# Optimization experiments

Measured on AMD Instinct MI355X. Metric: run time of the kernel, lower is better.

## Reference

```python
import jax, jax.numpy as jnp
import numpy as np

N = [50000, 100000, 100000, 40000, 20000]  # cells per rank 0..4
C = 64
DEG = 8
N_LAYERS = 3
PAIRS = [(0,0),(1,1),(2,2),(3,3),(4,4),(0,1),(0,2),(0,3),(0,4),(1,2),(1,3),(1,4),(2,3),(2,4),(3,4)]
E_SIZES = [DEG * N[j] for (_, j) in PAIRS]
OFF = np.concatenate([[0], np.cumsum(E_SIZES)]).astype(np.int64)
IN1 = C * 5 * 4 + 4  # 5 ranks pooled x 4 aggregators + global features


def setup_inputs() -> dict:
    key = jax.random.key(0)
    ks = jax.random.split(key, 64)
    inp = {}
    for r in range(5):
        inp[f'x_{r}'] = jax.random.normal(ks[r], (N[r], C), jnp.float32)
    rows_l, cols_l = [], []
    for k, (i, j) in enumerate(PAIRS):
        E = E_SIZES[k]
        rows_l.append(jnp.sort(jax.random.randint(ks[5 + k], (E,), 0, N[j], jnp.int32)))
        cols_l.append(jax.random.randint(ks[25 + k], (E,), 0, N[i], jnp.int32))
    inp['rows'] = jnp.concatenate(rows_l)
    inp['cols'] = jnp.concatenate(cols_l)
    inp['vals'] = jax.random.uniform(ks[41], (int(OFF[-1]),), jnp.float32) * 0.1
    inp['global_feature'] = jax.random.normal(ks[42], (1, 4), jnp.float32)
    inp['W_hmc'] = jax.random.normal(ks[43], (N_LAYERS, 15, C, C), jnp.float32) * 0.05
    inp['fc1_w'] = jax.random.normal(ks[44], (IN1, 512), jnp.float32) * 0.02
    inp['fc1_b'] = jnp.zeros((512,), jnp.float32)
    inp['fc2_w'] = jax.random.normal(ks[45], (512, 128), jnp.float32) * 0.05
    inp['fc2_b'] = jnp.zeros((128,), jnp.float32)
    inp['fc3_w'] = jax.random.normal(ks[46], (128, 64), jnp.float32) * 0.05
    inp['fc3_b'] = jnp.zeros((64,), jnp.float32)
    inp['fc4_w'] = jax.random.normal(ks[47], (64, 2), jnp.float32) * 0.05
    inp['fc4_b'] = jnp.zeros((2,), jnp.float32)
    return inp


def _gagg(x):
    # torch: cat((avg, std(unbiased=False, zeros->1e-6), max, min), dim=1), keepdim
    var = jnp.var(x, axis=0)
    std = jnp.sqrt(jnp.where(var == 0, jnp.float32(1e-6), var))
    return jnp.concatenate([jnp.mean(x, axis=0), std, jnp.max(x, axis=0), jnp.min(x, axis=0)])[None, :]


def _hmc(xs, rows, cols, vals, W_hmc):
    for l in range(N_LAYERS):
        hs = [jnp.zeros((N[j], C), xs[0].dtype) for j in range(5)]
        for k, (i, j) in enumerate(PAIRS):
            s, e = int(OFF[k]), int(OFF[k + 1])
            t = xs[i] @ W_hmc[l, k]                      # [N_i, C] dense transform
            msg = t[cols[s:e]] * vals[s:e, None]         # [E_k, C] irregular gather
            hs[j] = hs[j] + jax.ops.segment_sum(msg, rows[s:e], num_segments=N[j])
        if l > 1:  # residual_flag and layer_num > 1
            hs = [h + x for h, x in zip(hs, xs)]
        xs = [jax.nn.relu(h) for h in hs]
    return xs


def reference(x_0, x_1, x_2, x_3, x_4, rows, cols, vals, global_feature, W_hmc,
              fc1_w, fc1_b, fc2_w, fc2_b, fc3_w, fc3_b, fc4_w, fc4_b):
    xs = _hmc([x_0, x_1, x_2, x_3, x_4], rows, cols, vals, W_hmc)
    pooled = jnp.concatenate([_gagg(x) for x in xs] + [global_feature[:, :4]], axis=1)  # [1, IN1]
    h = jax.nn.relu(pooled @ fc1_w + fc1_b)
    h = jax.nn.relu(h @ fc2_w + fc2_b)
    h = jax.nn.relu(h @ fc3_w + fc3_b)
    out = h @ fc4_w + fc4_b
    half = out.shape[1] // 2
    return jnp.concatenate([out[:, :half], jnp.square(out[:, half:])], axis=1)
```

## Files before the change

kernel.cpp:

```cpp
#include <hip/hip_runtime.h>
#include <cstdint>
#include <cstddef>


namespace {

constexpr int NRr[5]  = {50000, 100000, 100000, 40000, 20000};
constexpr int PI[15]  = {0,1,2,3,4,0,0,0,0,1,1,1,2,2,3};
constexpr long long EOFF[15] = {0,400000,1200000,2000000,2320000,2480000,3280000,4080000,4400000,4560000,5360000,5680000,5840000,6160000,6320000};
constexpr int EK[15]  = {400000,800000,800000,320000,160000,800000,800000,320000,160000,800000,320000,160000,320000,160000,160000};
constexpr int POFF[15] = {0,50001,150002,250003,290004,310005,410006,510007,550008,570009,670010,710011,730012,770013,790014};
constexpr int PTR_TOT  = 810015;
constexpr int XOFF[5]  = {0,50000,150000,250000,290000};
constexpr int XROWS    = 310000;
constexpr int NPJ[5]    = {1,2,3,4,5};
constexpr int POJ[5][5] = {{0,0,0,0,0},{1,5,0,0,0},{2,6,9,0,0},{3,7,10,12,0},{4,8,11,13,14}};
constexpr int TCUM[6]  = {0,1250,3750,10000,16250,19375};
constexpr int TRANK[5] = {4,3,2,1,0};
constexpr int FUSED_BLOCKS = 19375;

constexpr size_t WS_B16IN = 0;
constexpr size_t WS_B16X  = 39680000;
constexpr size_t WS_B16Y  = 79360000;
constexpr size_t WS_PTR   = 119040000;
constexpr size_t WS_WT    = 122280064;
constexpr size_t WS_PSUM  = 122648704;
constexpr size_t WS_PSQ   = WS_PSUM + 327680;
constexpr size_t WS_PMAX  = WS_PSQ  + 327680;
constexpr size_t WS_PMIN  = WS_PMAX + 163840;
constexpr size_t WS_NEEDED = WS_PMIN + 163840;

struct XP  { const float* p[5]; };
struct XPB { const unsigned short* p[5]; };

}

typedef __attribute__((ext_vector_type(8))) short short8;
typedef __attribute__((ext_vector_type(4))) float f32x4;

static __device__ __forceinline__ unsigned int rne_bf16(float x) {
    unsigned int b = __float_as_uint(x);
    return (b + 0x7fffu + ((b >> 16) & 1u)) >> 16;
}
static __device__ __forceinline__ float4 bf16x4_to_f4(uint2 u) {
    float4 f;
    f.x = __uint_as_float(u.x << 16);
    f.y = __uint_as_float(u.x & 0xffff0000u);
    f.z = __uint_as_float(u.y << 16);
    f.w = __uint_as_float(u.y & 0xffff0000u);
    return f;
}
static __device__ __forceinline__ uint2 f4_to_bf16x4(float4 v) {
    uint2 st;
    st.x = rne_bf16(v.x) | (rne_bf16(v.y) << 16);
    st.y = rne_bf16(v.z) | (rne_bf16(v.w) << 16);
    return st;
}
static __device__ __forceinline__ void fma4(float4& a, float s, const float4& b) {
    a.x += s * b.x; a.y += s * b.y; a.z += s * b.z; a.w += s * b.w;
}
static __device__ __forceinline__ void fma8(float4& alo, float4& ahi, float s, uint4 g) {
    fma4(alo, s, bf16x4_to_f4(make_uint2(g.x, g.y)));
    fma4(ahi, s, bf16x4_to_f4(make_uint2(g.z, g.w)));
}
static __device__ __forceinline__ short8 pack_af(float4 lo, float4 hi) {
    uint2 pa = f4_to_bf16x4(lo);
    uint2 pb = f4_to_bf16x4(hi);
    short8 af;
    ((unsigned int*)&af)[0] = pa.x;
    ((unsigned int*)&af)[1] = pa.y;
    ((unsigned int*)&af)[2] = pb.x;
    ((unsigned int*)&af)[3] = pb.y;
    return af;
}

__global__ void k_diag(float* __restrict__ out, float v) {
    out[0] = v;
    out[1] = 0.f;
}

__global__ __launch_bounds__(256) void k_cvt(XP xin, unsigned short* __restrict__ b16) {
    int q = blockIdx.x * 256 + threadIdx.x;
    if (q >= XROWS * 16) return;
    int row = q >> 4;
    int rank = 0;
#pragma unroll
    for (int t = 1; t < 5; ++t) if (row >= XOFF[t]) rank = t;
    const float* src = xin.p[rank] + (size_t)(row - XOFF[rank]) * 64 + (q & 15) * 4;
    float4 v = *(const float4*)src;
    ((uint2*)b16)[q] = f4_to_bf16x4(v);
}

__global__ __launch_bounds__(256) void k_cvtw(const float* __restrict__ Wh,
                                              unsigned short* __restrict__ WT) {
    int tid = blockIdx.x * 256 + threadIdx.x;
    if (tid >= 3 * 15 * 4096) return;
    int lp = tid >> 12;
    int nk_ = tid & 4095;
    int n = nk_ >> 6;
    int k = nk_ & 63;
    float w = Wh[(size_t)lp * 4096 + k * 64 + n];
    WT[tid] = (unsigned short)rne_bf16(w);
}

__global__ __launch_bounds__(256) void k_ptr(const int* __restrict__ rows,
                                             int* __restrict__ rptr) {
    int tid = blockIdx.x * 256 + threadIdx.x;
    if (tid >= PTR_TOT) return;
    int k = 0;
#pragma unroll
    for (int t = 1; t < 15; ++t) if (tid >= POFF[t]) k = t;
    int r = tid - POFF[k];
    const int* rb = rows + EOFF[k];
    int lo = 0, hi = EK[k];
    while (lo < hi) {
        int mid = (lo + hi) >> 1;
        if (rb[mid] < r) lo = mid + 1; else hi = mid;
    }
    rptr[tid] = lo;
}

__global__ __launch_bounds__(64, 6) void k_fused(XPB xp,
                                                 const int* __restrict__ cols,
                                                 const float* __restrict__ vals,
                                                 const int* __restrict__ rptr,
                                                 const unsigned short* __restrict__ WT,
                                                 unsigned short* __restrict__ xout,
                                                 int layer) {
    __shared__ float C[16 * 65];

    int b = blockIdx.x;
    int seg = 0;
#pragma unroll
    for (int t = 1; t < 5; ++t) if (b >= TCUM[t]) seg = t;
    int j  = TRANK[seg];
    int r0 = (b - TCUM[seg]) * 16;

    int lane = threadIdx.x;
    int m    = lane & 15;
    int quad = lane >> 4;
    int s8   = quad * 8;

    f32x4 d0 = {0.f,0.f,0.f,0.f};
    f32x4 d1 = d0, d2 = d0, d3 = d0;

    const unsigned short* WTl = WT + (size_t)layer * 15 * 4096;
    int nk = NPJ[j];
    for (int kc = 0; kc < nk; ++kc) {
        int pk = POJ[j][kc];
        const unsigned short* __restrict__ xsrc = xp.p[PI[pk]];
        const int*   __restrict__ cb = cols + EOFF[pk];
        const float* __restrict__ vb = vals + EOFF[pk];
        const int*   __restrict__ rp = rptr + POFF[pk];

        int ps = rp[r0 + m];
        int pe = rp[r0 + m + 1];
        float4 a0lo = make_float4(0.f,0.f,0.f,0.f), a0hi = a0lo;
        float4 a1lo = a0lo, a1hi = a0lo;
        int e = ps;
        for (; e + 1 < pe; e += 2) {
            int   c0 = cb[e];
            int   c1 = cb[e + 1];
            float v0 = vb[e];
            float v1 = vb[e + 1];
            const unsigned short* r0p = xsrc + (size_t)c0 * 64;
            const unsigned short* r1p = xsrc + (size_t)c1 * 64;
            uint4 g00 = *(const uint4*)(r0p + s8);
            uint4 g01 = *(const uint4*)(r0p + 32 + s8);
            uint4 g10 = *(const uint4*)(r1p + s8);
            uint4 g11 = *(const uint4*)(r1p + 32 + s8);
            fma8(a0lo, a0hi, v0, g00);
            fma8(a1lo, a1hi, v0, g01);
            fma8(a0lo, a0hi, v1, g10);
            fma8(a1lo, a1hi, v1, g11);
        }
        if (e < pe) {
            int   c0 = cb[e];
            float v0 = vb[e];
            const unsigned short* r0p = xsrc + (size_t)c0 * 64;
            uint4 g00 = *(const uint4*)(r0p + s8);
            uint4 g01 = *(const uint4*)(r0p + 32 + s8);
            fma8(a0lo, a0hi, v0, g00);
            fma8(a1lo, a1hi, v0, g01);
        }
        short8 af0 = pack_af(a0lo, a0hi);
        short8 af1 = pack_af(a1lo, a1hi);

        const unsigned short* Wp = WTl + pk * 4096;
        short8 b00 = *(const short8*)(Wp + ( 0 + m) * 64 + s8);
        short8 b10 = *(const short8*)(Wp + (16 + m) * 64 + s8);
        short8 b20 = *(const short8*)(Wp + (32 + m) * 64 + s8);
        short8 b30 = *(const short8*)(Wp + (48 + m) * 64 + s8);
        d0 = __builtin_amdgcn_mfma_f32_16x16x32_bf16(af0, b00, d0, 0, 0, 0);
        d1 = __builtin_amdgcn_mfma_f32_16x16x32_bf16(af0, b10, d1, 0, 0, 0);
        d2 = __builtin_amdgcn_mfma_f32_16x16x32_bf16(af0, b20, d2, 0, 0, 0);
        d3 = __builtin_amdgcn_mfma_f32_16x16x32_bf16(af0, b30, d3, 0, 0, 0);
        short8 b01 = *(const short8*)(Wp + ( 0 + m) * 64 + 32 + s8);
        short8 b11 = *(const short8*)(Wp + (16 + m) * 64 + 32 + s8);
        short8 b21 = *(const short8*)(Wp + (32 + m) * 64 + 32 + s8);
        short8 b31 = *(const short8*)(Wp + (48 + m) * 64 + 32 + s8);
        d0 = __builtin_amdgcn_mfma_f32_16x16x32_bf16(af1, b01, d0, 0, 0, 0);
        d1 = __builtin_amdgcn_mfma_f32_16x16x32_bf16(af1, b11, d1, 0, 0, 0);
        d2 = __builtin_amdgcn_mfma_f32_16x16x32_bf16(af1, b21, d2, 0, 0, 0);
        d3 = __builtin_amdgcn_mfma_f32_16x16x32_bf16(af1, b31, d3, 0, 0, 0);
    }

#pragma unroll
    for (int g = 0; g < 4; ++g) {
        C[(quad * 4 + g) * 65 +  0 + m] = d0[g];
        C[(quad * 4 + g) * 65 + 16 + m] = d1[g];
        C[(quad * 4 + g) * 65 + 32 + m] = d2[g];
        C[(quad * 4 + g) * 65 + 48 + m] = d3[g];
    }
    __builtin_amdgcn_s_waitcnt(0);

    int row = lane >> 2;
    int qs  = lane & 3;
    const float* Cr = C + row * 65 + qs * 16;
    float4 v0 = *(const float4*)(Cr + 0);
    float4 v1 = *(const float4*)(Cr + 4);
    float4 v2 = *(const float4*)(Cr + 8);
    float4 v3 = *(const float4*)(Cr + 12);
    if (layer == 2) {
        const uint4* res = (const uint4*)(xp.p[j] + (size_t)(r0 + row) * 64 + qs * 16);
        uint4 ra = res[0];
        uint4 rb = res[1];
        float4 o0 = bf16x4_to_f4(make_uint2(ra.x, ra.y));
        float4 o1 = bf16x4_to_f4(make_uint2(ra.z, ra.w));
        float4 o2 = bf16x4_to_f4(make_uint2(rb.x, rb.y));
        float4 o3 = bf16x4_to_f4(make_uint2(rb.z, rb.w));
        v0.x += o0.x; v0.y += o0.y; v0.z += o0.z; v0.w += o0.w;
        v1.x += o1.x; v1.y += o1.y; v1.z += o1.z; v1.w += o1.w;
        v2.x += o2.x; v2.y += o2.y; v2.z += o2.z; v2.w += o2.w;
        v3.x += o3.x; v3.y += o3.y; v3.z += o3.z; v3.w += o3.w;
    }
    v0.x = fmaxf(v0.x, 0.f); v0.y = fmaxf(v0.y, 0.f); v0.z = fmaxf(v0.z, 0.f); v0.w = fmaxf(v0.w, 0.f);
    v1.x = fmaxf(v1.x, 0.f); v1.y = fmaxf(v1.y, 0.f); v1.z = fmaxf(v1.z, 0.f); v1.w = fmaxf(v1.w, 0.f);
    v2.x = fmaxf(v2.x, 0.f); v2.y = fmaxf(v2.y, 0.f); v2.z = fmaxf(v2.z, 0.f); v2.w = fmaxf(v2.w, 0.f);
    v3.x = fmaxf(v3.x, 0.f); v3.y = fmaxf(v3.y, 0.f); v3.z = fmaxf(v3.z, 0.f); v3.w = fmaxf(v3.w, 0.f);
    uint2 s0 = f4_to_bf16x4(v0);
    uint2 s1 = f4_to_bf16x4(v1);
    uint2 s2 = f4_to_bf16x4(v2);
    uint2 s3 = f4_to_bf16x4(v3);
    uint4* dst = (uint4*)(xout + (size_t)(XOFF[j] + r0 + row) * 64 + qs * 16);
    dst[0] = make_uint4(s0.x, s0.y, s1.x, s1.y);
    dst[1] = make_uint4(s2.x, s2.y, s3.x, s3.y);
}

__global__ __launch_bounds__(256) void k_pool1(const unsigned short* __restrict__ xs,
                                               double* __restrict__ psum,
                                               double* __restrict__ psq,
                                               float* __restrict__ pmax,
                                               float* __restrict__ pmin) {
    int rank = blockIdx.x >> 7;
    int blk  = blockIdx.x & 127;
    int c    = threadIdx.x & 63;
    int sub  = threadIdx.x >> 6;
    int N = NRr[rank];
    const unsigned short* xb = xs + (size_t)XOFF[rank] * 64;
    double s = 0.0, q = 0.0;
    float mx = -3.4e38f, mn = 3.4e38f;
    for (int r = blk * 4 + sub; r < N; r += 512) {
        float v = __uint_as_float(((unsigned int)xb[(size_t)r * 64 + c]) << 16);
        s += v; q += (double)v * (double)v;
        mx = fmaxf(mx, v); mn = fminf(mn, v);
    }
    __shared__ double ls[4][64], lq[4][64];
    __shared__ float lmx[4][64], lmn[4][64];
    ls[sub][c] = s; lq[sub][c] = q; lmx[sub][c] = mx; lmn[sub][c] = mn;
    __syncthreads();
    if (sub == 0) {
#pragma unroll
        for (int t = 1; t < 4; ++t) {
            s += ls[t][c]; q += lq[t][c];
            mx = fmaxf(mx, lmx[t][c]); mn = fminf(mn, lmn[t][c]);
        }
        int idx = (rank * 128 + blk) * 64 + c;
        psum[idx] = s; psq[idx] = q; pmax[idx] = mx; pmin[idx] = mn;
    }
}

__global__ __launch_bounds__(512) void k_tail(const double* __restrict__ psum,
                                              const double* __restrict__ psq,
                                              const float* __restrict__ pmax,
                                              const float* __restrict__ pmin,
                                              const float* __restrict__ gf,
                                              const float* __restrict__ w1, const float* __restrict__ b1,
                                              const float* __restrict__ w2, const float* __restrict__ b2,
                                              const float* __restrict__ w3, const float* __restrict__ b3,
                                              const float* __restrict__ w4, const float* __restrict__ b4,
                                              float* __restrict__ out) {
    __shared__ float sp[1284];
    __shared__ float h1[512];
    __shared__ float h2[128];
    __shared__ float h3[64];
    int tid = threadIdx.x;
    if (tid < 320) {
        int rank = tid >> 6;
        int c    = tid & 63;
        double s = 0.0, q = 0.0;
        float mx = -3.4e38f, mn = 3.4e38f;
        for (int b = 0; b < 128; ++b) {
            int idx = (rank * 128 + b) * 64 + c;
            s += psum[idx]; q += psq[idx];
            mx = fmaxf(mx, pmax[idx]); mn = fminf(mn, pmin[idx]);
        }
        double N = (double)NRr[rank];
        double mean = s / N;
        double var  = q / N - mean * mean;
        if (var < 0.0) var = 0.0;
        double sd = sqrt(var == 0.0 ? 1e-6 : var);
        sp[rank * 256 + c]       = (float)mean;
        sp[rank * 256 + 64 + c]  = (float)sd;
        sp[rank * 256 + 128 + c] = mx;
        sp[rank * 256 + 192 + c] = mn;
        if (rank == 0 && c < 4) sp[1280 + c] = gf[c];
    }
    __syncthreads();
    {
        float a = 0.f;
        for (int k2 = 0; k2 < 1284; ++k2) a += sp[k2] * w1[k2 * 512 + tid];
        h1[tid] = fmaxf(a + b1[tid], 0.f);
    }
    __syncthreads();
    if (tid < 128) {
        float a = 0.f;
        for (int k2 = 0; k2 < 512; ++k2) a += h1[k2] * w2[k2 * 128 + tid];
        h2[tid] = fmaxf(a + b2[tid], 0.f);
    }
    __syncthreads();
    if (tid < 64) {
        float a = 0.f;
        for (int k2 = 0; k2 < 128; ++k2) a += h2[k2] * w3[k2 * 64 + tid];
        h3[tid] = fmaxf(a + b3[tid], 0.f);
    }
    __syncthreads();
    if (tid < 2) {
        float a = 0.f;
        for (int k2 = 0; k2 < 64; ++k2) a += h3[k2] * w4[k2 * 2 + tid];
        a += b4[tid];
        if (tid == 1) a = a * a;
        out[tid] = a;
    }
}

extern "C" void kernel_launch(void* const* d_in, const int* in_sizes, int n_in,
                              void* d_out, int out_size, void* d_ws, size_t ws_size,
                              hipStream_t stream) {
    if (ws_size < WS_NEEDED) {
        hipLaunchKernelGGL(k_diag, dim3(1), dim3(1), 0, stream,
                           (float*)d_out, (float)(ws_size >> 20));
        return;
    }

    const float* x0   = (const float*)d_in[0];
    const float* x1   = (const float*)d_in[1];
    const float* x2   = (const float*)d_in[2];
    const float* x3   = (const float*)d_in[3];
    const float* x4   = (const float*)d_in[4];
    const int*   rows = (const int*)d_in[5];
    const int*   cols = (const int*)d_in[6];
    const float* vals = (const float*)d_in[7];
    const float* gf   = (const float*)d_in[8];
    const float* Wh   = (const float*)d_in[9];
    const float* w1   = (const float*)d_in[10];
    const float* b1   = (const float*)d_in[11];
    const float* w2   = (const float*)d_in[12];
    const float* b2   = (const float*)d_in[13];
    const float* w3   = (const float*)d_in[14];
    const float* b3   = (const float*)d_in[15];
    const float* w4   = (const float*)d_in[16];
    const float* b4   = (const float*)d_in[17];

    char* ws = (char*)d_ws;
    unsigned short* b16in = (unsigned short*)(ws + WS_B16IN);
    unsigned short* b16x  = (unsigned short*)(ws + WS_B16X);
    unsigned short* b16y  = (unsigned short*)(ws + WS_B16Y);
    int*    rptr   = (int*)(ws + WS_PTR);
    unsigned short* WT = (unsigned short*)(ws + WS_WT);
    double* psum   = (double*)(ws + WS_PSUM);
    double* psq    = (double*)(ws + WS_PSQ);
    float*  pmax   = (float*)(ws + WS_PMAX);
    float*  pmin   = (float*)(ws + WS_PMIN);

    XP xp_in; xp_in.p[0] = x0; xp_in.p[1] = x1; xp_in.p[2] = x2; xp_in.p[3] = x3; xp_in.p[4] = x4;
    hipLaunchKernelGGL(k_cvt, dim3((XROWS * 16 + 255) / 256), dim3(256), 0, stream, xp_in, b16in);
    hipLaunchKernelGGL(k_cvtw, dim3((3 * 15 * 4096 + 255) / 256), dim3(256), 0, stream, Wh, WT);
    hipLaunchKernelGGL(k_ptr, dim3((PTR_TOT + 255) / 256), dim3(256), 0, stream, rows, rptr);

    XPB xb_in, xb_x, xb_y;
    for (int i = 0; i < 5; ++i) {
        xb_in.p[i] = b16in + (size_t)XOFF[i] * 64;
        xb_x.p[i]  = b16x  + (size_t)XOFF[i] * 64;
        xb_y.p[i]  = b16y  + (size_t)XOFF[i] * 64;
    }

    hipLaunchKernelGGL(k_fused, dim3(FUSED_BLOCKS), dim3(64), 0, stream,
                       xb_in, cols, vals, rptr, WT, b16x, 0);
    hipLaunchKernelGGL(k_fused, dim3(FUSED_BLOCKS), dim3(64), 0, stream,
                       xb_x, cols, vals, rptr, WT, b16y, 1);
    hipLaunchKernelGGL(k_fused, dim3(FUSED_BLOCKS), dim3(64), 0, stream,
                       xb_y, cols, vals, rptr, WT, b16x, 2);

    hipLaunchKernelGGL(k_pool1, dim3(5 * 128), dim3(256), 0, stream, b16x, psum, psq, pmax, pmin);
    hipLaunchKernelGGL(k_tail, dim3(1), dim3(512), 0, stream, psum, psq, pmax, pmin, gf,
                       w1, b1, w2, b2, w3, b3, w4, b4, (float*)d_out);
}
```

Baseline: 929.5 us.

## Pack four waves per fused block, unroll gather by four, split MLP tail

```diff
diff --git a/kernel.cpp b/kernel.cpp
--- a/kernel.cpp
+++ b/kernel.cpp
@@ -19,16 +19,21 @@
 constexpr int TRANK[5] = {4,3,2,1,0};
 constexpr int FUSED_BLOCKS = 19375;
 
+constexpr int PB = 32;
+
 constexpr size_t WS_B16IN = 0;
 constexpr size_t WS_B16X  = 39680000;
 constexpr size_t WS_B16Y  = 79360000;
 constexpr size_t WS_PTR   = 119040000;
 constexpr size_t WS_WT    = 122280064;
 constexpr size_t WS_PSUM  = 122648704;
-constexpr size_t WS_PSQ   = WS_PSUM + 327680;
-constexpr size_t WS_PMAX  = WS_PSQ  + 327680;
-constexpr size_t WS_PMIN  = WS_PMAX + 163840;
-constexpr size_t WS_NEEDED = WS_PMIN + 163840;
+constexpr size_t WS_PSQ   = WS_PSUM + (size_t)5*PB*64*8;
+constexpr size_t WS_PMAX  = WS_PSQ  + (size_t)5*PB*64*8;
+constexpr size_t WS_PMIN  = WS_PMAX + (size_t)5*PB*64*4;
+constexpr size_t WS_SP    = WS_PMIN + (size_t)5*PB*64*4;
+constexpr size_t WS_H1    = WS_SP + 5136;
+constexpr size_t WS_H2    = WS_H1 + 2048;
+constexpr size_t WS_NEEDED = WS_H2 + 512;
 
 struct XP  { const float* p[5]; };
 struct XPB { const unsigned short* p[5]; };
@@ -120,23 +125,27 @@
     rptr[tid] = lo;
 }
 
-__global__ __launch_bounds__(64, 6) void k_fused(XPB xp,
-                                                 const int* __restrict__ cols,
-                                                 const float* __restrict__ vals,
-                                                 const int* __restrict__ rptr,
-                                                 const unsigned short* __restrict__ WT,
-                                                 unsigned short* __restrict__ xout,
-                                                 int layer) {
-    __shared__ float C[16 * 65];
-
-    int b = blockIdx.x;
+__global__ __launch_bounds__(256, 6) void k_fused(XPB xp,
+                                                  const int* __restrict__ cols,
+                                                  const float* __restrict__ vals,
+                                                  const int* __restrict__ rptr,
+                                                  const unsigned short* __restrict__ WT,
+                                                  unsigned short* __restrict__ xout,
+                                                  int layer) {
+    __shared__ float C[4][16 * 65];
+
+    int wid  = threadIdx.x >> 6;
+    int lane = threadIdx.x & 63;
+    int b = blockIdx.x * 4 + wid;
+    if (b >= FUSED_BLOCKS) return;
+    float* Cw = &C[wid][0];
+
     int seg = 0;
 #pragma unroll
     for (int t = 1; t < 5; ++t) if (b >= TCUM[t]) seg = t;
     int j  = TRANK[seg];
     int r0 = (b - TCUM[seg]) * 16;
 
-    int lane = threadIdx.x;
     int m    = lane & 15;
     int quad = lane >> 4;
     int s8   = quad * 8;
@@ -158,28 +167,59 @@
         float4 a0lo = make_float4(0.f,0.f,0.f,0.f), a0hi = a0lo;
         float4 a1lo = a0lo, a1hi = a0lo;
         int e = ps;
-        for (; e + 1 < pe; e += 2) {
+        for (; e + 3 < pe; e += 4) {
+            int   c0 = cb[e];
+            int   c1 = cb[e + 1];
+            int   c2 = cb[e + 2];
+            int   c3 = cb[e + 3];
+            float v0 = vb[e];
+            float v1 = vb[e + 1];
+            float v2 = vb[e + 2];
+            float v3 = vb[e + 3];
+            const unsigned short* p0 = xsrc + (size_t)c0 * 64;
+            const unsigned short* p1 = xsrc + (size_t)c1 * 64;
+            const unsigned short* p2 = xsrc + (size_t)c2 * 64;
+            const unsigned short* p3 = xsrc + (size_t)c3 * 64;
+            uint4 g00 = *(const uint4*)(p0 + s8);
+            uint4 g01 = *(const uint4*)(p0 + 32 + s8);
+            uint4 g10 = *(const uint4*)(p1 + s8);
+            uint4 g11 = *(const uint4*)(p1 + 32 + s8);
+            uint4 g20 = *(const uint4*)(p2 + s8);
+            uint4 g21 = *(const uint4*)(p2 + 32 + s8);
+            uint4 g30 = *(const uint4*)(p3 + s8);
+            uint4 g31 = *(const uint4*)(p3 + 32 + s8);
+            fma8(a0lo, a0hi, v0, g00);
+            fma8(a1lo, a1hi, v0, g01);
+            fma8(a0lo, a0hi, v1, g10);
+            fma8(a1lo, a1hi, v1, g11);
+            fma8(a0lo, a0hi, v2, g20);
+            fma8(a1lo, a1hi, v2, g21);
+            fma8(a0lo, a0hi, v3, g30);
+            fma8(a1lo, a1hi, v3, g31);
+        }
+        if (e + 1 < pe) {
             int   c0 = cb[e];
             int   c1 = cb[e + 1];
             float v0 = vb[e];
             float v1 = vb[e + 1];
-            const unsigned short* r0p = xsrc + (size_t)c0 * 64;
-            const unsigned short* r1p = xsrc + (size_t)c1 * 64;
-            uint4 g00 = *(const uint4*)(r0p + s8);
-            uint4 g01 = *(const uint4*)(r0p + 32 + s8);
-            uint4 g10 = *(const uint4*)(r1p + s8);
-            uint4 g11 = *(const uint4*)(r1p + 32 + s8);
+            const unsigned short* p0 = xsrc + (size_t)c0 * 64;
+            const unsigned short* p1 = xsrc + (size_t)c1 * 64;
+            uint4 g00 = *(const uint4*)(p0 + s8);
+            uint4 g01 = *(const uint4*)(p0 + 32 + s8);
+            uint4 g10 = *(const uint4*)(p1 + s8);
+            uint4 g11 = *(const uint4*)(p1 + 32 + s8);
             fma8(a0lo, a0hi, v0, g00);
             fma8(a1lo, a1hi, v0, g01);
             fma8(a0lo, a0hi, v1, g10);
             fma8(a1lo, a1hi, v1, g11);
+            e += 2;
         }
         if (e < pe) {
             int   c0 = cb[e];
             float v0 = vb[e];
-            const unsigned short* r0p = xsrc + (size_t)c0 * 64;
-            uint4 g00 = *(const uint4*)(r0p + s8);
-            uint4 g01 = *(const uint4*)(r0p + 32 + s8);
+            const unsigned short* p0 = xsrc + (size_t)c0 * 64;
+            uint4 g00 = *(const uint4*)(p0 + s8);
+            uint4 g01 = *(const uint4*)(p0 + 32 + s8);
             fma8(a0lo, a0hi, v0, g00);
             fma8(a1lo, a1hi, v0, g01);
         }
@@ -207,16 +247,16 @@
 
 #pragma unroll
     for (int g = 0; g < 4; ++g) {
-        C[(quad * 4 + g) * 65 +  0 + m] = d0[g];
-        C[(quad * 4 + g) * 65 + 16 + m] = d1[g];
-        C[(quad * 4 + g) * 65 + 32 + m] = d2[g];
-        C[(quad * 4 + g) * 65 + 48 + m] = d3[g];
+        Cw[(quad * 4 + g) * 65 +  0 + m] = d0[g];
+        Cw[(quad * 4 + g) * 65 + 16 + m] = d1[g];
+        Cw[(quad * 4 + g) * 65 + 32 + m] = d2[g];
+        Cw[(quad * 4 + g) * 65 + 48 + m] = d3[g];
     }
     __builtin_amdgcn_s_waitcnt(0);
 
     int row = lane >> 2;
     int qs  = lane & 3;
-    const float* Cr = C + row * 65 + qs * 16;
+    const float* Cr = Cw + row * 65 + qs * 16;
     float4 v0 = *(const float4*)(Cr + 0);
     float4 v1 = *(const float4*)(Cr + 4);
     float4 v2 = *(const float4*)(Cr + 8);
@@ -252,15 +292,15 @@
                                                double* __restrict__ psq,
                                                float* __restrict__ pmax,
                                                float* __restrict__ pmin) {
-    int rank = blockIdx.x >> 7;
-    int blk  = blockIdx.x & 127;
+    int rank = blockIdx.x / PB;
+    int blk  = blockIdx.x % PB;
     int c    = threadIdx.x & 63;
     int sub  = threadIdx.x >> 6;
     int N = NRr[rank];
     const unsigned short* xb = xs + (size_t)XOFF[rank] * 64;
     double s = 0.0, q = 0.0;
     float mx = -3.4e38f, mn = 3.4e38f;
-    for (int r = blk * 4 + sub; r < N; r += 512) {
+    for (int r = blk * 4 + sub; r < N; r += PB * 4) {
         float v = __uint_as_float(((unsigned int)xb[(size_t)r * 64 + c]) << 16);
         s += v; q += (double)v * (double)v;
         mx = fmaxf(mx, v); mn = fminf(mn, v);
@@ -275,72 +315,102 @@
             s += ls[t][c]; q += lq[t][c];
             mx = fmaxf(mx, lmx[t][c]); mn = fminf(mn, lmn[t][c]);
         }
-        int idx = (rank * 128 + blk) * 64 + c;
+        int idx = (rank * PB + blk) * 64 + c;
         psum[idx] = s; psq[idx] = q; pmax[idx] = mx; pmin[idx] = mn;
     }
 }
 
-__global__ __launch_bounds__(512) void k_tail(const double* __restrict__ psum,
-                                              const double* __restrict__ psq,
-                                              const float* __restrict__ pmax,
-                                              const float* __restrict__ pmin,
-                                              const float* __restrict__ gf,
-                                              const float* __restrict__ w1, const float* __restrict__ b1,
-                                              const float* __restrict__ w2, const float* __restrict__ b2,
-                                              const float* __restrict__ w3, const float* __restrict__ b3,
-                                              const float* __restrict__ w4, const float* __restrict__ b4,
-                                              float* __restrict__ out) {
-    __shared__ float sp[1284];
-    __shared__ float h1[512];
-    __shared__ float h2[128];
+__global__ __launch_bounds__(320) void k_pool2(const double* __restrict__ psum,
+                                               const double* __restrict__ psq,
+                                               const float* __restrict__ pmax,
+                                               const float* __restrict__ pmin,
+                                               const float* __restrict__ gf,
+                                               float* __restrict__ sp) {
+    int tid = threadIdx.x;
+    int rank = tid >> 6;
+    int c    = tid & 63;
+    double s = 0.0, q = 0.0;
+    float mx = -3.4e38f, mn = 3.4e38f;
+    for (int b = 0; b < PB; ++b) {
+        int idx = (rank * PB + b) * 64 + c;
+        s += psum[idx]; q += psq[idx];
+        mx = fmaxf(mx, pmax[idx]); mn = fminf(mn, pmin[idx]);
+    }
+    double N = (double)NRr[rank];
+    double mean = s / N;
+    double var  = q / N - mean * mean;
+    if (var < 0.0) var = 0.0;
+    double sd = sqrt(var == 0.0 ? 1e-6 : var);
+    sp[rank * 256 + c]       = (float)mean;
+    sp[rank * 256 + 64 + c]  = (float)sd;
+    sp[rank * 256 + 128 + c] = mx;
+    sp[rank * 256 + 192 + c] = mn;
+    if (rank == 0 && c < 4) sp[1280 + c] = gf[c];
+}
+
+__global__ __launch_bounds__(256) void k_fc1(const float* __restrict__ sp,
+                                             const float* __restrict__ w1,
+                                             const float* __restrict__ b1,
+                                             float* __restrict__ h1) {
+    __shared__ float red[16][17];
+    int tid = threadIdx.x;
+    int oi = tid & 15;
+    int ks = tid >> 4;
+    int o = (blockIdx.x << 4) | oi;
+    float a = 0.f;
+    for (int k = ks; k < 1284; k += 16) a += sp[k] * w1[(size_t)k * 512 + o];
+    red[ks][oi] = a;
+    __syncthreads();
+    if (tid < 16) {
+        float s = 0.f;
+#pragma unroll
+        for (int t = 0; t < 16; ++t) s += red[t][tid];
+        int oo = (blockIdx.x << 4) | tid;
+        h1[oo] = fmaxf(s + b1[oo], 0.f);
+    }
+}
+
+__global__ __launch_bounds__(256) void k_fc2(const float* __restrict__ h1,
+                                             const float* __restrict__ w2,
+                                             const float* __restrict__ b2,
+                                             float* __restrict__ h2) {
+    __shared__ float red[16][17];
+    int tid = threadIdx.x;
+    int oi = tid & 15;
+    int ks = tid >> 4;
+    int o = (blockIdx.x << 4) | oi;
+    float a = 0.f;
+    for (int k = ks; k < 512; k += 16) a += h1[k] * w2[(size_t)k * 128 + o];
+    red[ks][oi] = a;
+    __syncthreads();
+    if (tid < 16) {
+        float s = 0.f;
+#pragma unroll
+        for (int t = 0; t < 16; ++t) s += red[t][tid];
+        int oo = (blockIdx.x << 4) | tid;
+        h2[oo] = fmaxf(s + b2[oo], 0.f);
+    }
+}
+
+__global__ __launch_bounds__(64) void k_rest(const float* __restrict__ h2,
+                                             const float* __restrict__ w3,
+                                             const float* __restrict__ b3,
+                                             const float* __restrict__ w4,
+                                             const float* __restrict__ b4,
+                                             float* __restrict__ out) {
     __shared__ float h3[64];
     int tid = threadIdx.x;
-    if (tid < 320) {
-        int rank = tid >> 6;
-        int c    = tid & 63;
-        double s = 0.0, q = 0.0;
-        float mx = -3.4e38f, mn = 3.4e38f;
-        for (int b = 0; b < 128; ++b) {
-            int idx = (rank * 128 + b) * 64 + c;
-            s += psum[idx]; q += psq[idx];
-            mx = fmaxf(mx, pmax[idx]); mn = fminf(mn, pmin[idx]);
-        }
-        double N = (double)NRr[rank];
-        double mean = s / N;
-        double var  = q / N - mean * mean;
-        if (var < 0.0) var = 0.0;
-        double sd = sqrt(var == 0.0 ? 1e-6 : var);
-        sp[rank * 256 + c]       = (float)mean;
-        sp[rank * 256 + 64 + c]  = (float)sd;
-        sp[rank * 256 + 128 + c] = mx;
-        sp[rank * 256 + 192 + c] = mn;
-        if (rank == 0 && c < 4) sp[1280 + c] = gf[c];
-    }
-    __syncthreads();
-    {
-        float a = 0.f;
-        for (int k2 = 0; k2 < 1284; ++k2) a += sp[k2] * w1[k2 * 512 + tid];
-        h1[tid] = fmaxf(a + b1[tid], 0.f);
-    }
-    __syncthreads();
-    if (tid < 128) {
-        float a = 0.f;
-        for (int k2 = 0; k2 < 512; ++k2) a += h1[k2] * w2[k2 * 128 + tid];
-        h2[tid] = fmaxf(a + b2[tid], 0.f);
-    }
-    __syncthreads();
-    if (tid < 64) {
-        float a = 0.f;
-        for (int k2 = 0; k2 < 128; ++k2) a += h2[k2] * w3[k2 * 64 + tid];
-        h3[tid] = fmaxf(a + b3[tid], 0.f);
-    }
+    float a = 0.f;
+    for (int k = 0; k < 128; ++k) a += h2[k] * w3[k * 64 + tid];
+    h3[tid] = fmaxf(a + b3[tid], 0.f);
     __syncthreads();
     if (tid < 2) {
-        float a = 0.f;
-        for (int k2 = 0; k2 < 64; ++k2) a += h3[k2] * w4[k2 * 2 + tid];
-        a += b4[tid];
-        if (tid == 1) a = a * a;
-        out[tid] = a;
+        float s = 0.f;
+#pragma unroll
+        for (int k = 0; k < 64; ++k) s += h3[k] * w4[k * 2 + tid];
+        s += b4[tid];
+        if (tid == 1) s = s * s;
+        out[tid] = s;
     }
 }
 
@@ -382,6 +452,9 @@
     double* psq    = (double*)(ws + WS_PSQ);
     float*  pmax   = (float*)(ws + WS_PMAX);
     float*  pmin   = (float*)(ws + WS_PMIN);
+    float*  sp     = (float*)(ws + WS_SP);
+    float*  h1     = (float*)(ws + WS_H1);
+    float*  h2     = (float*)(ws + WS_H2);
 
     XP xp_in; xp_in.p[0] = x0; xp_in.p[1] = x1; xp_in.p[2] = x2; xp_in.p[3] = x3; xp_in.p[4] = x4;
     hipLaunchKernelGGL(k_cvt, dim3((XROWS * 16 + 255) / 256), dim3(256), 0, stream, xp_in, b16in);
@@ -395,14 +468,17 @@
         xb_y.p[i]  = b16y  + (size_t)XOFF[i] * 64;
     }
 
-    hipLaunchKernelGGL(k_fused, dim3(FUSED_BLOCKS), dim3(64), 0, stream,
+    int fgrid = (FUSED_BLOCKS + 3) / 4;
+    hipLaunchKernelGGL(k_fused, dim3(fgrid), dim3(256), 0, stream,
                        xb_in, cols, vals, rptr, WT, b16x, 0);
-    hipLaunchKernelGGL(k_fused, dim3(FUSED_BLOCKS), dim3(64), 0, stream,
+    hipLaunchKernelGGL(k_fused, dim3(fgrid), dim3(256), 0, stream,
                        xb_x, cols, vals, rptr, WT, b16y, 1);
-    hipLaunchKernelGGL(k_fused, dim3(FUSED_BLOCKS), dim3(64), 0, stream,
+    hipLaunchKernelGGL(k_fused, dim3(fgrid), dim3(256), 0, stream,
                        xb_y, cols, vals, rptr, WT, b16x, 2);
 
-    hipLaunchKernelGGL(k_pool1, dim3(5 * 128), dim3(256), 0, stream, b16x, psum, psq, pmax, pmin);
-    hipLaunchKernelGGL(k_tail, dim3(1), dim3(512), 0, stream, psum, psq, pmax, pmin, gf,
-                       w1, b1, w2, b2, w3, b3, w4, b4, (float*)d_out);
-}
+    hipLaunchKernelGGL(k_pool1, dim3(5 * PB), dim3(256), 0, stream, b16x, psum, psq, pmax, pmin);
+    hipLaunchKernelGGL(k_pool2, dim3(1), dim3(320), 0, stream, psum, psq, pmax, pmin, gf, sp);
+    hipLaunchKernelGGL(k_fc1, dim3(32), dim3(256), 0, stream, sp, w1, b1, h1);
+    hipLaunchKernelGGL(k_fc2, dim3(8), dim3(256), 0, stream, h1, w2, b2, h2);
+    hipLaunchKernelGGL(k_rest, dim3(1), dim3(64), 0, stream, h2, w3, b3, w4, b4, (float*)d_out);
+}
```

New measurement: 1.269 ms. 36.5% more time.
